# Kernel optimization log

Measured on AMD Instinct MI355X. Metric: run time of the kernel, lower is better.

## Reference

```python
import jax, jax.numpy as jnp
import numpy as np

SEQ_LEN, INPUT_DIM, HIDDEN_DIM, OUTPUT_DIM = 1024, 128, 256, 128
BATCH = 256


def setup_inputs() -> dict:
    key = jax.random.key(0)
    ks = jax.random.split(key, 12)
    s_x = 1.0 / np.sqrt(INPUT_DIM)
    s_h = 1.0 / np.sqrt(HIDDEN_DIM)
    def lin(k, fan_in, shape, scale):
        return jax.random.uniform(k, shape, jnp.float32, -scale, scale)
    inp = {"x": jax.random.normal(ks[0], (BATCH, SEQ_LEN, INPUT_DIM), jnp.float32)}
    names = ["g", "i", "f", "o"]
    for j, n in enumerate(names):
        inp[f"W{n}x"] = lin(ks[1 + 2 * j], INPUT_DIM, (HIDDEN_DIM, INPUT_DIM), s_x)
        inp[f"b{n}x"] = lin(jax.random.fold_in(ks[1 + 2 * j], 1), INPUT_DIM, (HIDDEN_DIM,), s_x)
        inp[f"W{n}h"] = lin(ks[2 + 2 * j], HIDDEN_DIM, (HIDDEN_DIM, HIDDEN_DIM), s_h)
    inp["Wp"] = lin(ks[9], HIDDEN_DIM, (OUTPUT_DIM, HIDDEN_DIM), s_h)
    inp["bp"] = lin(ks[10], HIDDEN_DIM, (OUTPUT_DIM,), s_h)
    return inp


def reference(x, Wgx, bgx, Wgh, Wix, bix, Wih, Wfx, bfx, Wfh, Wox, box, Woh, Wp, bp):
    B = x.shape[0]
    H = Wgh.shape[0]
    # Precompute all input projections in one batched GEMM per gate: (B,T,H)
    gx = jnp.einsum('bti,hi->bth', x, Wgx) + bgx
    ix = jnp.einsum('bti,hi->bth', x, Wix) + bix
    fx = jnp.einsum('bti,hi->bth', x, Wfx) + bfx
    ox = jnp.einsum('bti,hi->bth', x, Wox) + box
    xs = jnp.stack([gx, ix, fx, ox], axis=0).transpose(2, 0, 1, 3)  # (T,4,B,H)

    def step(carry, x_t):
        h, c = carry
        gx_t, ix_t, fx_t, ox_t = x_t[0], x_t[1], x_t[2], x_t[3]
        g = jnp.tanh(gx_t + h @ Wgh.T)
        i = jax.nn.sigmoid(ix_t + h @ Wih.T)
        f = jax.nn.sigmoid(fx_t + h @ Wfh.T)
        o = jax.nn.sigmoid(ox_t + h @ Woh.T)
        c = g * i + c * f
        h = jnp.tanh(c) * o
        return (h, c), None

    h0 = jnp.zeros((B, H), x.dtype)
    c0 = jnp.zeros((B, H), x.dtype)
    (h_T, _), _ = jax.lax.scan(step, (h0, c0), xs)
    return h_T @ Wp.T + bp
```

## Files before the change

### kernel.cpp

```cpp
#include <hip/hip_runtime.h>
#include <hip/hip_fp16.h>

#define TSEQ 1024
#define NBATCH 256
#define HD 256
#define ID 128
#define ODIM 128

typedef _Float16 f16;
typedef _Float16 f16x8 __attribute__((ext_vector_type(8)));
typedef float f32x4 __attribute__((ext_vector_type(4)));

__global__ void pack_weights(
    const float* __restrict__ Wgh, const float* __restrict__ Wih,
    const float* __restrict__ Wfh, const float* __restrict__ Woh,
    const float* __restrict__ Wgx, const float* __restrict__ Wix,
    const float* __restrict__ Wfx, const float* __restrict__ Wox,
    const float* __restrict__ bgx, const float* __restrict__ bix,
    const float* __restrict__ bfx, const float* __restrict__ box,
    f16* __restrict__ Whcat, f16* __restrict__ Wxcat, float* __restrict__ bcat)
{
    const int np = blockIdx.x;
    const int g  = (np >> 6) & 3;
    const int j  = np >> 8;
    const int uu = np & 63;
    const int u  = j * 64 + uu;
    const float* Wh = (g == 0) ? Wgh : (g == 1) ? Wih : (g == 2) ? Wfh : Woh;
    const float* Wx = (g == 0) ? Wgx : (g == 1) ? Wix : (g == 2) ? Wfx : Wox;
    const float* bx = (g == 0) ? bgx : (g == 1) ? bix : (g == 2) ? bfx : box;
    const int k = threadIdx.x;
    Whcat[np * 256 + k] = (f16)Wh[u * 256 + k];
    if (k < ID) Wxcat[np * ID + k] = (f16)Wx[u * ID + k];
    if (k == 0) bcat[np] = bx[u];
}

__global__ __launch_bounds__(256, 1) void lstm_rec(
    const float* __restrict__ x,
    const f16* __restrict__ Whcat,
    const f16* __restrict__ Wxcat,
    const float* __restrict__ bcat,
    f16* __restrict__ hbuf,
    float* __restrict__ hT,
    int* __restrict__ flags)
{
    const int tid  = threadIdx.x;
    const int lane = tid & 63;
    const int w    = tid >> 6;
    const int q    = lane >> 4;
    const int n    = lane & 15;
    const int bid  = blockIdx.x;
    const int grp  = bid >> 2;
    const int j    = bid & 3;
    const int b0   = grp * 16;

    f16x8 wh[4][8];
    f16x8 wx[4][4];
    float bias[4];
#pragma unroll
    for (int g = 0; g < 4; ++g) {
        const int row = j * 256 + g * 64 + w * 16 + n;
        bias[g] = bcat[row];
#pragma unroll
        for (int kk = 0; kk < 8; ++kk)
            wh[g][kk] = *(const f16x8*)&Whcat[row * 256 + kk * 32 + q * 8];
#pragma unroll
        for (int k4 = 0; k4 < 4; ++k4)
            wx[g][k4] = *(const f16x8*)&Wxcat[row * ID + k4 * 32 + q * 8];
    }

    float c[4] = {0.f, 0.f, 0.f, 0.f};
    const int uglob    = j * 64 + w * 16 + n;
    const int myslot   = (grp * 16 + j * 4 + w) * 64;
    const int pollslot = (grp * 16 + tid) * 64;

    const float* xrow = &x[(size_t)(b0 + n) * TSEQ * ID];
    float4 xr[8];
#pragma unroll
    for (int k4 = 0; k4 < 4; ++k4) {
        xr[k4 * 2]     = *(const float4*)&xrow[k4 * 32 + q * 8];
        xr[k4 * 2 + 1] = *(const float4*)&xrow[k4 * 32 + q * 8 + 4];
    }

    for (int t = 0; t < TSEQ; ++t) {
        f16x8 xa[4];
#pragma unroll
        for (int k4 = 0; k4 < 4; ++k4) {
            const float* f0 = (const float*)&xr[k4 * 2];
            const float* f1 = (const float*)&xr[k4 * 2 + 1];
#pragma unroll
            for (int e = 0; e < 4; ++e) {
                xa[k4][e]     = (f16)f0[e];
                xa[k4][4 + e] = (f16)f1[e];
            }
        }
        if (t + 1 < TSEQ) {
            const float* xp = &xrow[(size_t)(t + 1) * ID];
#pragma unroll
            for (int k4 = 0; k4 < 4; ++k4) {
                xr[k4 * 2]     = *(const float4*)&xp[k4 * 32 + q * 8];
                xr[k4 * 2 + 1] = *(const float4*)&xp[k4 * 32 + q * 8 + 4];
            }
        }

        f32x4 acc[4];
#pragma unroll
        for (int g = 0; g < 4; ++g) {
            f32x4 av = {bias[g], bias[g], bias[g], bias[g]};
            acc[g] = av;
        }
#pragma unroll
        for (int k4 = 0; k4 < 4; ++k4)
#pragma unroll
            for (int g = 0; g < 4; ++g)
                acc[g] = __builtin_amdgcn_mfma_f32_16x16x32_f16(xa[k4], wx[g][k4], acc[g], 0, 0, 0);

        if (t > 0) {
            if (tid < 16) {
                while (__hip_atomic_load(&flags[pollslot], __ATOMIC_RELAXED,
                                         __HIP_MEMORY_SCOPE_AGENT) < t)
                    __builtin_amdgcn_s_sleep(1);
            }
            __syncthreads();
            const unsigned long long* hp = (const unsigned long long*)
                &hbuf[(size_t)(((t - 1) & 1) * NBATCH + b0 + n) * HD];
            f16x8 ha[8];
#pragma unroll
            for (int kk = 0; kk < 8; ++kk) {
                union { unsigned long long u[2]; f16x8 v; } hu;
                hu.u[0] = __hip_atomic_load(hp + kk * 8 + q * 2,     __ATOMIC_RELAXED,
                                            __HIP_MEMORY_SCOPE_AGENT);
                hu.u[1] = __hip_atomic_load(hp + kk * 8 + q * 2 + 1, __ATOMIC_RELAXED,
                                            __HIP_MEMORY_SCOPE_AGENT);
                ha[kk] = hu.v;
            }
#pragma unroll
            for (int kk = 0; kk < 8; ++kk)
#pragma unroll
                for (int g = 0; g < 4; ++g)
                    acc[g] = __builtin_amdgcn_mfma_f32_16x16x32_f16(ha[kk], wh[g][kk], acc[g], 0, 0, 0);
        }

#pragma unroll
        for (int r = 0; r < 4; ++r) {
            const float gp_ = acc[0][r], ip_ = acc[1][r], fp_ = acc[2][r], op_ = acc[3][r];
            const float gg = 1.f - 2.f / (1.f + __expf(2.f * gp_));
            const float ii = 1.f / (1.f + __expf(-ip_));
            const float ff = 1.f / (1.f + __expf(-fp_));
            const float oo = 1.f / (1.f + __expf(-op_));
            c[r] = gg * ii + c[r] * ff;
            const float hh = (1.f - 2.f / (1.f + __expf(2.f * c[r]))) * oo;
            const int b = b0 + q * 4 + r;
            if (t < TSEQ - 1) {
                union { _Float16 f; unsigned short s; } cv;
                cv.f = (_Float16)hh;
                __hip_atomic_store((unsigned short*)&hbuf[(size_t)((t & 1) * NBATCH + b) * HD + uglob],
                                   cv.s, __ATOMIC_RELAXED, __HIP_MEMORY_SCOPE_AGENT);
            } else {
                hT[(size_t)b * HD + uglob] = hh;
            }
        }

        if (t < TSEQ - 1) {
            __atomic_signal_fence(__ATOMIC_SEQ_CST);
            __builtin_amdgcn_s_waitcnt(0x0F70);
            __atomic_signal_fence(__ATOMIC_SEQ_CST);
            if (lane == 0)
                __hip_atomic_store(&flags[myslot], t + 1, __ATOMIC_RELAXED,
                                   __HIP_MEMORY_SCOPE_AGENT);
        }
    }
}

__global__ void out_proj(const float* __restrict__ hT, const float* __restrict__ Wp,
                         const float* __restrict__ bp, float* __restrict__ out)
{
    const int b = blockIdx.x;
    const int o = threadIdx.x;
    __shared__ float hrow[HD];
    for (int u = threadIdx.x; u < HD; u += ODIM) hrow[u] = hT[b * HD + u];
    __syncthreads();
    float s = bp[o];
    const float* wr = &Wp[o * HD];
#pragma unroll 8
    for (int u = 0; u < HD; ++u) s += hrow[u] * wr[u];
    out[b * ODIM + o] = s;
}

extern "C" void kernel_launch(void* const* d_in, const int* in_sizes, int n_in,
                              void* d_out, int out_size, void* d_ws, size_t ws_size,
                              hipStream_t stream) {
    const float* x   = (const float*)d_in[0];
    const float* Wgx = (const float*)d_in[1];
    const float* bgx = (const float*)d_in[2];
    const float* Wgh = (const float*)d_in[3];
    const float* Wix = (const float*)d_in[4];
    const float* bix = (const float*)d_in[5];
    const float* Wih = (const float*)d_in[6];
    const float* Wfx = (const float*)d_in[7];
    const float* bfx = (const float*)d_in[8];
    const float* Wfh = (const float*)d_in[9];
    const float* Wox = (const float*)d_in[10];
    const float* box = (const float*)d_in[11];
    const float* Woh = (const float*)d_in[12];
    const float* Wp  = (const float*)d_in[13];
    const float* bp  = (const float*)d_in[14];
    float* out = (float*)d_out;

    char* ws = (char*)d_ws;
    f16*   Whcat = (f16*)(ws);
    f16*   Wxcat = (f16*)(ws + 524288);
    float* bcat  = (float*)(ws + 786432);
    f16*   hbuf  = (f16*)(ws + 790528);
    float* hT    = (float*)(ws + 1052672);
    int*   flags = (int*)(ws + 1314816);

    hipMemsetAsync(flags, 0, 256 * 64 * sizeof(int), stream);
    pack_weights<<<1024, 256, 0, stream>>>(Wgh, Wih, Wfh, Woh,
                                           Wgx, Wix, Wfx, Wox,
                                           bgx, bix, bfx, box,
                                           Whcat, Wxcat, bcat);
    lstm_rec<<<64, 256, 0, stream>>>(x, Whcat, Wxcat, bcat, hbuf, hT, flags);
    out_proj<<<NBATCH, ODIM, 0, stream>>>(hT, Wp, bp, out);
}
```

Before: 5.174 ms.

## Stage hidden state in LDS for coalesced stores, pack flags, defer x prefetch

Each step's new hidden values are first written to a shared-memory tile. After a block barrier, each thread publishes them with one 64-bit atomic store, replacing four scattered 16-bit atomic stores per thread. The per-wave ready flags are packed into consecutive ints instead of being padded 64 ints apart, and the memset shrinks to match. The next-step x prefetch now happens after the flag store, so the vmcnt wait before signalling no longer waits on those loads. The trade-offs are an extra barrier on the critical path and flags that now share cache lines.

```diff
diff --git a/kernel.cpp b/kernel.cpp
--- a/kernel.cpp
+++ b/kernel.cpp
@@ -10,6 +10,7 @@
 typedef _Float16 f16;
 typedef _Float16 f16x8 __attribute__((ext_vector_type(8)));
 typedef float f32x4 __attribute__((ext_vector_type(4)));
+typedef unsigned long long ull;
 
 __global__ void pack_weights(
     const float* __restrict__ Wgh, const float* __restrict__ Wih,
@@ -43,6 +44,8 @@
     float* __restrict__ hT,
     int* __restrict__ flags)
 {
+    __shared__ f16 h_st[16 * 64];
+
     const int tid  = threadIdx.x;
     const int lane = tid & 63;
     const int w    = tid >> 6;
@@ -69,9 +72,12 @@
     }
 
     float c[4] = {0.f, 0.f, 0.f, 0.f};
-    const int uglob    = j * 64 + w * 16 + n;
-    const int myslot   = (grp * 16 + j * 4 + w) * 64;
-    const int pollslot = (grp * 16 + tid) * 64;
+    const int uglob = j * 64 + w * 16 + n;
+    const int myflag   = grp * 16 + j * 4 + w;
+    const int pollflag = grp * 16 + tid;
+
+    const int rr = tid >> 4;
+    const int cc = tid & 15;
 
     const float* xrow = &x[(size_t)(b0 + n) * TSEQ * ID];
     float4 xr[8];
@@ -93,14 +99,6 @@
                 xa[k4][4 + e] = (f16)f1[e];
             }
         }
-        if (t + 1 < TSEQ) {
-            const float* xp = &xrow[(size_t)(t + 1) * ID];
-#pragma unroll
-            for (int k4 = 0; k4 < 4; ++k4) {
-                xr[k4 * 2]     = *(const float4*)&xp[k4 * 32 + q * 8];
-                xr[k4 * 2 + 1] = *(const float4*)&xp[k4 * 32 + q * 8 + 4];
-            }
-        }
 
         f32x4 acc[4];
 #pragma unroll
@@ -116,17 +114,17 @@
 
         if (t > 0) {
             if (tid < 16) {
-                while (__hip_atomic_load(&flags[pollslot], __ATOMIC_RELAXED,
+                while (__hip_atomic_load(&flags[pollflag], __ATOMIC_RELAXED,
                                          __HIP_MEMORY_SCOPE_AGENT) < t)
                     __builtin_amdgcn_s_sleep(1);
             }
             __syncthreads();
-            const unsigned long long* hp = (const unsigned long long*)
+            const ull* hp = (const ull*)
                 &hbuf[(size_t)(((t - 1) & 1) * NBATCH + b0 + n) * HD];
             f16x8 ha[8];
 #pragma unroll
             for (int kk = 0; kk < 8; ++kk) {
-                union { unsigned long long u[2]; f16x8 v; } hu;
+                union { ull u[2]; f16x8 v; } hu;
                 hu.u[0] = __hip_atomic_load(hp + kk * 8 + q * 2,     __ATOMIC_RELAXED,
                                             __HIP_MEMORY_SCOPE_AGENT);
                 hu.u[1] = __hip_atomic_load(hp + kk * 8 + q * 2 + 1, __ATOMIC_RELAXED,
@@ -140,6 +138,7 @@
                     acc[g] = __builtin_amdgcn_mfma_f32_16x16x32_f16(ha[kk], wh[g][kk], acc[g], 0, 0, 0);
         }
 
+        float hh[4];
 #pragma unroll
         for (int r = 0; r < 4; ++r) {
             const float gp_ = acc[0][r], ip_ = acc[1][r], fp_ = acc[2][r], op_ = acc[3][r];
@@ -148,25 +147,35 @@
             const float ff = 1.f / (1.f + __expf(-fp_));
             const float oo = 1.f / (1.f + __expf(-op_));
             c[r] = gg * ii + c[r] * ff;
-            const float hh = (1.f - 2.f / (1.f + __expf(2.f * c[r]))) * oo;
-            const int b = b0 + q * 4 + r;
-            if (t < TSEQ - 1) {
-                union { _Float16 f; unsigned short s; } cv;
-                cv.f = (_Float16)hh;
-                __hip_atomic_store((unsigned short*)&hbuf[(size_t)((t & 1) * NBATCH + b) * HD + uglob],
-                                   cv.s, __ATOMIC_RELAXED, __HIP_MEMORY_SCOPE_AGENT);
-            } else {
-                hT[(size_t)b * HD + uglob] = hh;
-            }
+            hh[r] = (1.f - 2.f / (1.f + __expf(2.f * c[r]))) * oo;
         }
 
         if (t < TSEQ - 1) {
+#pragma unroll
+            for (int r = 0; r < 4; ++r)
+                h_st[(q * 4 + r) * 64 + w * 16 + n] = (f16)hh[r];
+            __syncthreads();
+            {
+                ull v = *(const ull*)&h_st[rr * 64 + cc * 4];
+                ull* dst = (ull*)&hbuf[(size_t)((t & 1) * NBATCH + b0 + rr) * HD + j * 64 + cc * 4];
+                __hip_atomic_store(dst, v, __ATOMIC_RELAXED, __HIP_MEMORY_SCOPE_AGENT);
+            }
             __atomic_signal_fence(__ATOMIC_SEQ_CST);
             __builtin_amdgcn_s_waitcnt(0x0F70);
             __atomic_signal_fence(__ATOMIC_SEQ_CST);
             if (lane == 0)
-                __hip_atomic_store(&flags[myslot], t + 1, __ATOMIC_RELAXED,
+                __hip_atomic_store(&flags[myflag], t + 1, __ATOMIC_RELAXED,
                                    __HIP_MEMORY_SCOPE_AGENT);
+            const float* xp = &xrow[(size_t)(t + 1) * ID];
+#pragma unroll
+            for (int k4 = 0; k4 < 4; ++k4) {
+                xr[k4 * 2]     = *(const float4*)&xp[k4 * 32 + q * 8];
+                xr[k4 * 2 + 1] = *(const float4*)&xp[k4 * 32 + q * 8 + 4];
+            }
+        } else {
+#pragma unroll
+            for (int r = 0; r < 4; ++r)
+                hT[(size_t)(b0 + q * 4 + r) * HD + uglob] = hh[r];
         }
     }
 }
@@ -214,7 +223,7 @@
     float* hT    = (float*)(ws + 1052672);
     int*   flags = (int*)(ws + 1314816);
 
-    hipMemsetAsync(flags, 0, 256 * 64 * sizeof(int), stream);
+    hipMemsetAsync(flags, 0, 16 * 16 * sizeof(int), stream);
     pack_weights<<<1024, 256, 0, stream>>>(Wgh, Wih, Wfh, Woh,
                                            Wgx, Wix, Wfx, Wox,
                                            bgx, bix, bfx, box,
```

New measurement: 5.378 ms. 3.9% more time.
